# Kernel optimization log

Hardware: AMD Instinct MI355X
Metric: run time of the kernel (lower is better)

The kernel has to match this reference:

```python
import jax, jax.numpy as jnp
import numpy as np

# ---- fixed 16-atom graph topology from OrbECG.__init__ (flag_cg_global == 0) ----
EDGE1 = np.array([0, 0, 1, 2, 2, 3, 4, 5, 6, 8, 8, 9, 10, 11, 11, 13, 14])
EDGE2 = np.array([1, 4, 2, 3, 5, 4, 12, 6, 7, 9, 12, 10, 11, 12, 13, 14, 15])
EDGE_LIST = [[1, 4], [0, 2], [1, 3, 5], [2, 4], [0, 3, 12], [2, 6], [5, 7], [5, 6],
             [9, 12], [8, 10], [9, 11], [10, 12, 13], [4, 8, 11], [11, 14], [13, 15], [13, 14]]

def _build_pairs():
    eps, ni = [], []
    for node_idx, conn in enumerate(EDGE_LIST):
        for i in range(len(conn)):
            for j in range(i + 1, len(conn)):
                eps.append((conn[i], conn[j]))
                ni.append(node_idx)
    return np.array(eps), np.array(ni)

EDGE_PAIRS, NODE_IDX = _build_pairs()          # (24,2), (24,)
CROSS_SCALE = np.array([-0.25, 0.25], np.float32)
SIGMA_LIST = np.array([0.4, 0.8, 1.2], np.float32)
NUM_ATOMS = 16
N1 = NUM_ATOMS + len(EDGE1)                    # 33 (atoms + bond midpoints)
N2 = len(CROSS_SCALE) * len(EDGE_PAIRS)        # 48 cross points
BLOCK = N1 + N2                                # 81 per sigma block
NUM_BASIS = len(SIGMA_LIST) * BLOCK            # 243
NUM_BEADS = 8
NUM_ENC = 128
BATCH = 1024


def make_opposite_blocks(C):
    """Faithful to OrbECG.make_opposite_blocks: within each sigma block, the n2
    (cross-point) columns are tied in pairs: even col keeps gradient, odd col = -even (detached).
    All other columns come from a detached clone."""
    cols = jnp.arange(NUM_BASIS)
    bpos = cols % BLOCK
    off = bpos - N1
    even_mask = (bpos >= N1) & (off % 2 == 0)
    odd_mask = (bpos >= N1) & (off % 2 == 1)
    shifted = jnp.roll(C, 1, axis=-1)  # value at previous column (the paired even col)
    base = jax.lax.stop_gradient(C)
    out = jnp.where(even_mask, C, base)
    out = jnp.where(odd_mask, -jax.lax.stop_gradient(shifted), out)
    return out


def setup_inputs() -> dict:
    key = jax.random.key(0)
    ks = jax.random.split(key, 8)
    pos = jax.random.normal(ks[0], (BATCH, NUM_ATOMS, 3), jnp.float32)
    cg_ref = 0.01 * jax.random.normal(ks[1], (1, NUM_BEADS, NUM_BASIS), jnp.float32)
    sigma_param = jnp.zeros((len(SIGMA_LIST),), jnp.float32)
    # SoftEncoder(enc_ovl): num_bins=128, bin_min=-1, bin_max=1, sigma=0.2
    centers = jnp.linspace(-1.0, 1.0, NUM_ENC)[None, :].astype(jnp.float32)
    enc_weight = centers / (0.2 ** 2)
    enc_bias = -0.5 * (centers / 0.2) ** 2
    mu_proj = jnp.linspace(-2.5, 3.0, NUM_ENC)[:, None].astype(jnp.float32)
    lr_proj = jnp.array([3.5], jnp.float32)
    b = 1.0 / np.sqrt(NUM_ENC)
    def lin(k, o, i):
        k1, k2 = jax.random.split(k)
        return (jax.random.uniform(k1, (o, i), jnp.float32, -b, b),
                jax.random.uniform(k2, (o,), jnp.float32, -b, b))
    W1, b1 = lin(ks[2], NUM_ENC, NUM_ENC)
    W2, b2 = lin(ks[3], NUM_ENC, NUM_ENC)
    W3, b3 = lin(ks[4], NUM_ENC, NUM_ENC)
    return {"pos": pos, "cg_ref": cg_ref, "sigma_param": sigma_param,
            "enc_weight": enc_weight, "enc_bias": enc_bias, "mu_proj": mu_proj,
            "lr_proj": lr_proj, "W1": W1, "b1": b1, "W2": W2, "b2": b2, "W3": W3, "b3": b3}


def reference(pos, cg_ref, sigma_param, enc_weight, enc_bias, mu_proj, lr_proj,
              W1, b1, W2, b2, W3, b3):
    B = pos.shape[0]
    e1 = jnp.asarray(EDGE1); e2 = jnp.asarray(EDGE2)
    ep = jnp.asarray(EDGE_PAIRS); ni = jnp.asarray(NODE_IDX)
    # --- reference Gaussian centers: atoms, bond midpoints (basis_list=[0.5]), cross points ---
    atom = pos                                             # (B,16,3)
    bond = 0.5 * (pos[:, e1] + pos[:, e2])                 # (B,17,3)
    center = pos[:, ni]                                    # (B,24,3)
    diff = pos[:, ep[:, 0]] - pos[:, ep[:, 1]]             # (B,24,3)
    cross = center[:, :, None, :] + jnp.asarray(CROSS_SCALE)[None, None, :, None] * diff[:, :, None, :]
    pts_blk = jnp.concatenate([atom, bond, cross.reshape(B, N2, 3)], axis=1)  # (B,81,3)
    pts = jnp.tile(pts_blk, (1, len(SIGMA_LIST), 1))        # (B,243,3)
    sig = jnp.repeat(jnp.asarray(SIGMA_LIST) * jnp.exp(sigma_param), BLOCK)   # (243,)
    # --- pairwise Gaussian overlap matrix S (B,243,243) ---
    d2 = jnp.sum((pts[:, :, None, :] - pts[:, None, :, :]) ** 2, axis=-1)
    s2 = sig[:, None] ** 2 + sig[None, :] ** 2
    S = (2.0 * sig[:, None] * sig[None, :] / s2) ** 1.5 * jnp.exp(-d2 / (2.0 * s2))
    # --- bead-bead overlaps via CG coefficients (antisymmetrized cross columns) ---
    C = make_opposite_blocks(cg_ref[0])                     # (8,243)
    T = jnp.einsum('bij,qj->biq', S, C)
    ovl = jnp.einsum('pi,biq->bpq', C, T)                   # (B,8,8)
    # --- soft encode overlaps, MLP prediction, project onto mu grid ---
    x = ovl.reshape(-1, 1)                                  # (B*64,1)
    e = jax.nn.softmax(enc_weight * x + enc_bias, axis=1)   # (B*64,128)
    h = jax.nn.relu(e @ W1.T + b1)
    h = jax.nn.relu(h @ W2.T + b2)
    h = h @ W3.T + b3
    p = jax.nn.softmax(h, axis=1)
    mu = p @ mu_proj                                        # (B*64,1)
    return lr_proj[0] * mu.reshape(B, NUM_BEADS, NUM_BEADS)
```

## Files before the change

### kernel.cpp

```cpp
#include <hip/hip_runtime.h>

#define NT 256
#define NBATCH 1024
#define NOUT 65536

#if __has_builtin(__builtin_amdgcn_exp2f)
#define EXP2(x) __builtin_amdgcn_exp2f(x)
#else
#define EXP2(x) exp2f(x)
#endif

__constant__ int c_e1[17] = {0,0,1,2,2,3,4,5,6,8,8,9,10,11,11,13,14};
__constant__ int c_e2[17] = {1,4,2,3,5,4,12,6,7,9,12,10,11,12,13,14,15};
__constant__ int c_p0[24] = {1,0,1,1,3,2,0,0,3,2,5,5,9,8,9,10,10,12,4,4,8,11,13,13};
__constant__ int c_p1[24] = {4,2,3,5,5,4,3,12,12,6,7,6,12,10,11,11,13,13,8,11,11,14,15,14};
__constant__ int c_ni[24] = {0,1,2,2,2,3,4,4,4,5,6,7,8,9,10,11,11,11,12,12,12,13,14,15};

__constant__ int c_pa[6]   = {0,0,0,1,1,2};
__constant__ int c_pb[6]   = {0,1,2,1,2,2};
__constant__ int c_diag[6] = {1,0,0,1,0,1};

__global__ __launch_bounds__(256, 6)
void k_ovl(const float* __restrict__ pos, const float* __restrict__ cg,
           const float* __restrict__ sigp, float* __restrict__ xout,
           float* __restrict__ bmin, float* __restrict__ bmax) {
  __shared__ __align__(16) float smem[6216];
  float* posS          = smem;
  float (*P4)[4]       = (float(*)[4])   (smem + 48);
  float (*CT)[81][8]   = (float(*)[81][8])(smem + 372);
  float (*Vall)[81][8] = (float(*)[81][8])(smem + 2316);
  float* cInv          = smem + 6204;
  float* cLgp          = smem + 6210;
  float (*red16)[65]   = (float(*)[65])  (smem + 2316);

  const int b = blockIdx.x;
  const int t = threadIdx.x;

  if (t < 48) posS[t] = pos[b * 48 + t];

  for (int idx = t; idx < 3 * 81 * 8; idx += 256) {
    int s = idx / 648;
    int rem = idx - s * 648;
    int j = rem >> 3, q = rem & 7;
    int col = s * 81 + j;
    int off = j - 33;
    float v;
    if (off >= 0 && (off & 1)) v = -cg[q * 243 + (col - 1)];
    else                       v =  cg[q * 243 + col];
    CT[s][j][q] = v;
  }

  if (t == 0) {
    float sg[3];
    sg[0] = 0.4f * __expf(sigp[0]);
    sg[1] = 0.8f * __expf(sigp[1]);
    sg[2] = 1.2f * __expf(sigp[2]);
    #pragma unroll
    for (int p = 0; p < 6; ++p) {
      float sa = sg[c_pa[p]], sb = sg[c_pb[p]];
      float s2 = sa * sa + sb * sb;
      float rr = 2.0f * sa * sb / s2;
      cLgp[p] = 1.5f * __log2f(rr) - (float)c_diag[p];
      cInv[p] = (-0.5f / s2) * 1.44269504088896f;
    }
  }
  __syncthreads();

  if (t < 81) {
    float x, y, z;
    if (t < 16) {
      x = posS[t * 3]; y = posS[t * 3 + 1]; z = posS[t * 3 + 2];
    } else if (t < 33) {
      int e = t - 16;
      int a0 = c_e1[e] * 3, a1 = c_e2[e] * 3;
      x = 0.5f * (posS[a0] + posS[a1]);
      y = 0.5f * (posS[a0 + 1] + posS[a1 + 1]);
      z = 0.5f * (posS[a0 + 2] + posS[a1 + 2]);
    } else {
      int k = (t - 33) >> 1, sgn = (t - 33) & 1;
      float sc = sgn ? 0.25f : -0.25f;
      int n = c_ni[k] * 3, a0 = c_p0[k] * 3, a1 = c_p1[k] * 3;
      x = posS[n]     + sc * (posS[a0]     - posS[a1]);
      y = posS[n + 1] + sc * (posS[a0 + 1] - posS[a1 + 1]);
      z = posS[n + 2] + sc * (posS[a0 + 2] - posS[a1 + 2]);
    }
    P4[t][0] = x; P4[t][1] = y; P4[t][2] = z;
    P4[t][3] = x * x + y * y + z * z;
  }
  __syncthreads();

  if (t < 246) {
    const int s = t / 41;
    const int st = t - s * 41;
    const int i0 = st * 2;
    const bool two = (st < 40);
    const int i1 = two ? i0 + 1 : i0;
    const int bb = c_pb[s];
    const float nInv = cInv[s];
    const float lgp  = cLgp[s];

    const float4 pA = *(const float4*)P4[i0];
    const float4 pB = *(const float4*)P4[i1];
    const float cA = fmaf(pA.w, nInv, lgp);
    const float cB = fmaf(pB.w, nInv, lgp);
    const float m2 = -2.0f * nInv;

    float v00=0,v01=0,v02=0,v03=0,v04=0,v05=0,v06=0,v07=0;
    float v10=0,v11=0,v12=0,v13=0,v14=0,v15=0,v16=0,v17=0;

    #pragma unroll 3
    for (int j = 0; j < 33; ++j) {
      const float4 pj = *(const float4*)P4[j];
      const float rj = pj.w * nInv;
      const float dA = pA.x * pj.x + pA.y * pj.y + pA.z * pj.z;
      const float dB = pB.x * pj.x + pB.y * pj.y + pB.z * pj.z;
      const float eA = EXP2(fmaf(m2, dA, cA + rj));
      const float eB = EXP2(fmaf(m2, dB, cB + rj));
      const float4 cb0 = *(const float4*)&CT[bb][j][0];
      const float4 cb1 = *(const float4*)&CT[bb][j][4];
      v00 = fmaf(eA, cb0.x, v00); v01 = fmaf(eA, cb0.y, v01);
      v02 = fmaf(eA, cb0.z, v02); v03 = fmaf(eA, cb0.w, v03);
      v04 = fmaf(eA, cb1.x, v04); v05 = fmaf(eA, cb1.y, v05);
      v06 = fmaf(eA, cb1.z, v06); v07 = fmaf(eA, cb1.w, v07);
      v10 = fmaf(eB, cb0.x, v10); v11 = fmaf(eB, cb0.y, v11);
      v12 = fmaf(eB, cb0.z, v12); v13 = fmaf(eB, cb0.w, v13);
      v14 = fmaf(eB, cb1.x, v14); v15 = fmaf(eB, cb1.y, v15);
      v16 = fmaf(eB, cb1.z, v16); v17 = fmaf(eB, cb1.w, v17);
    }

    for (int k = 0; k < 24; ++k) {
      const int jp = 33 + (k << 1);
      const float4 pp = *(const float4*)P4[jp];
      const float4 pm = *(const float4*)P4[jp + 1];
      const float rp = pp.w * nInv;
      const float rm = pm.w * nInv;
      const float dAp = pA.x * pp.x + pA.y * pp.y + pA.z * pp.z;
      const float dBp = pB.x * pp.x + pB.y * pp.y + pB.z * pp.z;
      const float dAm = pA.x * pm.x + pA.y * pm.y + pA.z * pm.z;
      const float dBm = pB.x * pm.x + pB.y * pm.y + pB.z * pm.z;
      const float gA = EXP2(fmaf(m2, dAp, cA + rp)) - EXP2(fmaf(m2, dAm, cA + rm));
      const float gB = EXP2(fmaf(m2, dBp, cB + rp)) - EXP2(fmaf(m2, dBm, cB + rm));
      const float4 cb0 = *(const float4*)&CT[bb][jp][0];
      const float4 cb1 = *(const float4*)&CT[bb][jp][4];
      v00 = fmaf(gA, cb0.x, v00); v01 = fmaf(gA, cb0.y, v01);
      v02 = fmaf(gA, cb0.z, v02); v03 = fmaf(gA, cb0.w, v03);
      v04 = fmaf(gA, cb1.x, v04); v05 = fmaf(gA, cb1.y, v05);
      v06 = fmaf(gA, cb1.z, v06); v07 = fmaf(gA, cb1.w, v07);
      v10 = fmaf(gB, cb0.x, v10); v11 = fmaf(gB, cb0.y, v11);
      v12 = fmaf(gB, cb0.z, v12); v13 = fmaf(gB, cb0.w, v13);
      v14 = fmaf(gB, cb1.x, v14); v15 = fmaf(gB, cb1.y, v15);
      v16 = fmaf(gB, cb1.z, v16); v17 = fmaf(gB, cb1.w, v17);
    }

    float4* vo = (float4*)&Vall[s][i0][0];
    vo[0] = make_float4(v00, v01, v02, v03);
    vo[1] = make_float4(v04, v05, v06, v07);
    if (two) {
      vo[2] = make_float4(v10, v11, v12, v13);
      vo[3] = make_float4(v14, v15, v16, v17);
    }
  }
  __syncthreads();

  float w00=0,w01=0,w02=0,w03=0, w10=0,w11=0,w12=0,w13=0;
  float w20=0,w21=0,w22=0,w23=0, w30=0,w31=0,w32=0,w33=0;
  const int ch = t & 15;
  if (t < 64) {
    const int pg = (t >> 5) & 1;
    const int qg = (t >> 4) & 1;
    const int ib = ch * 5;
    const int ie = (ch == 15) ? 81 : ib + 5;
    #pragma unroll
    for (int s = 0; s < 6; ++s) {
      const int lf = c_pa[s];
      for (int i = ib; i < ie; ++i) {
        const float4 ct = *(const float4*)&CT[lf][i][pg * 4];
        const float4 vv = *(const float4*)&Vall[s][i][qg * 4];
        w00 = fmaf(ct.x, vv.x, w00); w01 = fmaf(ct.x, vv.y, w01);
        w02 = fmaf(ct.x, vv.z, w02); w03 = fmaf(ct.x, vv.w, w03);
        w10 = fmaf(ct.y, vv.x, w10); w11 = fmaf(ct.y, vv.y, w11);
        w12 = fmaf(ct.y, vv.z, w12); w13 = fmaf(ct.y, vv.w, w13);
        w20 = fmaf(ct.z, vv.x, w20); w21 = fmaf(ct.z, vv.y, w21);
        w22 = fmaf(ct.z, vv.z, w22); w23 = fmaf(ct.z, vv.w, w23);
        w30 = fmaf(ct.w, vv.x, w30); w31 = fmaf(ct.w, vv.y, w31);
        w32 = fmaf(ct.w, vv.z, w32); w33 = fmaf(ct.w, vv.w, w33);
      }
    }
  }
  __syncthreads();
  if (t < 64) {
    const int pg = (t >> 5) & 1;
    const int qg = (t >> 4) & 1;
    const int base = pg * 32 + qg * 4;
    red16[ch][base + 0 * 8 + 0] = w00; red16[ch][base + 0 * 8 + 1] = w01;
    red16[ch][base + 0 * 8 + 2] = w02; red16[ch][base + 0 * 8 + 3] = w03;
    red16[ch][base + 1 * 8 + 0] = w10; red16[ch][base + 1 * 8 + 1] = w11;
    red16[ch][base + 1 * 8 + 2] = w12; red16[ch][base + 1 * 8 + 3] = w13;
    red16[ch][base + 2 * 8 + 0] = w20; red16[ch][base + 2 * 8 + 1] = w21;
    red16[ch][base + 2 * 8 + 2] = w22; red16[ch][base + 2 * 8 + 3] = w23;
    red16[ch][base + 3 * 8 + 0] = w30; red16[ch][base + 3 * 8 + 1] = w31;
    red16[ch][base + 3 * 8 + 2] = w32; red16[ch][base + 3 * 8 + 3] = w33;
  }
  __syncthreads();

  if (t < 64) {
    float ws = 0.0f;
    #pragma unroll
    for (int c = 0; c < 16; ++c) ws += red16[c][t];
    const float sym = __shfl(ws, ((t & 7) << 3) | (t >> 3));
    const float v = ws + sym;
    xout[b * 64 + t] = v;
    float vmin = v, vmax = v;
    #pragma unroll
    for (int off = 32; off; off >>= 1) {
      vmin = fminf(vmin, __shfl_down(vmin, off));
      vmax = fmaxf(vmax, __shfl_down(vmax, off));
    }
    if (t == 0) { bmin[b] = vmin; bmax[b] = vmax; }
  }
}

__device__ __forceinline__ float dot128(const float* __restrict__ W,
                                        const float* __restrict__ act, int t) {
  const float4* w4 = (const float4*)(W + (size_t)t * 128);
  const float4* a4 = (const float4*)act;
  float acc = 0.0f;
  #pragma unroll
  for (int kq = 0; kq < 32; ++kq) {
    float4 w = w4[kq];
    float4 a = a4[kq];
    acc += w.x * a.x + w.y * a.y + w.z * a.z + w.w * a.w;
  }
  return acc;
}

__global__ __launch_bounds__(128)
void k_table(const float* __restrict__ ew, const float* __restrict__ eb,
             const float* __restrict__ mup, const float* __restrict__ lrp,
             const float* __restrict__ W1, const float* __restrict__ b1,
             const float* __restrict__ W2, const float* __restrict__ b2,
             const float* __restrict__ W3, const float* __restrict__ b3,
             const float* __restrict__ bmin, const float* __restrict__ bmax,
             float* __restrict__ mmf, float* __restrict__ table) {
  __shared__ __align__(16) float actA[128];
  __shared__ __align__(16) float actB[128];
  __shared__ float red[2];
  __shared__ float red2[2];
  const int t = threadIdx.x;
  const int wv = t >> 6;

  float mn = 1e30f, mx = -1e30f;
  #pragma unroll
  for (int i = 0; i < 8; ++i) {
    mn = fminf(mn, bmin[t + i * 128]);
    mx = fmaxf(mx, bmax[t + i * 128]);
  }
  #pragma unroll
  for (int off = 32; off; off >>= 1) {
    mn = fminf(mn, __shfl_xor(mn, off));
    mx = fmaxf(mx, __shfl_xor(mx, off));
  }
  if ((t & 63) == 0) { red[wv] = mn; red2[wv] = mx; }
  __syncthreads();
  const float xmin = fminf(red[0], red[1]);
  const float xmax = fmaxf(red2[0], red2[1]);
  if (blockIdx.x == 0 && t == 0) { mmf[0] = xmin; mmf[1] = xmax; }
  __syncthreads();

  const float x = xmin + (xmax - xmin) * ((float)blockIdx.x / (float)(NT - 1));

  float lg = ew[t] * x + eb[t];
  float m = lg;
  #pragma unroll
  for (int off = 32; off; off >>= 1) m = fmaxf(m, __shfl_xor(m, off));
  if ((t & 63) == 0) red[wv] = m;
  __syncthreads();
  m = fmaxf(red[0], red[1]);
  float ev = __expf(lg - m);
  float s = ev;
  #pragma unroll
  for (int off = 32; off; off >>= 1) s += __shfl_xor(s, off);
  if ((t & 63) == 0) red2[wv] = s;
  __syncthreads();
  s = red2[0] + red2[1];
  actA[t] = ev / s;
  __syncthreads();

  float h = fmaxf(b1[t] + dot128(W1, actA, t), 0.0f);
  actB[t] = h;
  __syncthreads();
  h = fmaxf(b2[t] + dot128(W2, actB, t), 0.0f);
  actA[t] = h;
  __syncthreads();
  float h3 = b3[t] + dot128(W3, actA, t);

  float m3 = h3;
  #pragma unroll
  for (int off = 32; off; off >>= 1) m3 = fmaxf(m3, __shfl_xor(m3, off));
  __syncthreads();
  if ((t & 63) == 0) red[wv] = m3;
  __syncthreads();
  m3 = fmaxf(red[0], red[1]);
  float e3 = __expf(h3 - m3);
  float dn = e3;
  float nm = e3 * mup[t];
  #pragma unroll
  for (int off = 32; off; off >>= 1) {
    dn += __shfl_xor(dn, off);
    nm += __shfl_xor(nm, off);
  }
  __syncthreads();
  if ((t & 63) == 0) { red[wv] = dn; red2[wv] = nm; }
  __syncthreads();
  if (t == 0)
    table[blockIdx.x] = lrp[0] * ((red2[0] + red2[1]) / (red[0] + red[1]));
}

__global__ __launch_bounds__(256)
void k_interp(const float* __restrict__ xbuf, const float* __restrict__ table,
              const float* __restrict__ mmf, float* __restrict__ out, int n) {
  const int r = blockIdx.x * 256 + threadIdx.x;
  if (r >= n) return;
  const float xmin = mmf[0];
  const float xmax = mmf[1];
  const float range = xmax - xmin;
  const float scale = (range > 0.0f) ? (float)(NT - 1) / range : 0.0f;
  float p = (xbuf[r] - xmin) * scale;
  int i0 = (int)floorf(p);
  i0 = min(max(i0, 0), NT - 2);
  const float w = p - (float)i0;
  out[r] = table[i0] + w * (table[i0 + 1] - table[i0]);
}

extern "C" void kernel_launch(void* const* d_in, const int* in_sizes, int n_in,
                              void* d_out, int out_size, void* d_ws, size_t ws_size,
                              hipStream_t stream) {
  const float* pos  = (const float*)d_in[0];
  const float* cg   = (const float*)d_in[1];
  const float* sigp = (const float*)d_in[2];
  const float* ew   = (const float*)d_in[3];
  const float* eb   = (const float*)d_in[4];
  const float* mup  = (const float*)d_in[5];
  const float* lrp  = (const float*)d_in[6];
  const float* W1   = (const float*)d_in[7];
  const float* b1   = (const float*)d_in[8];
  const float* W2   = (const float*)d_in[9];
  const float* b2   = (const float*)d_in[10];
  const float* W3   = (const float*)d_in[11];
  const float* b3   = (const float*)d_in[12];
  float* out = (float*)d_out;

  float* mmf   = (float*)d_ws;
  float* xbuf  = (float*)d_ws + 16;
  float* table = xbuf + NOUT;
  float* bmin  = table + NT;
  float* bmax  = bmin + NBATCH;

  k_ovl<<<NBATCH, 256, 0, stream>>>(pos, cg, sigp, xbuf, bmin, bmax);
  k_table<<<NT, 128, 0, stream>>>(ew, eb, mup, lrp, W1, b1, W2, b2, W3, b3,
                                  bmin, bmax, mmf, table);
  k_interp<<<(NOUT + 255) / 256, 256, 0, stream>>>(xbuf, table, mmf, out, NOUT);
}
```

Baseline: 38.60 us.

## Split overlap kernel across two blocks per batch with fp16 shared buffers

Each batch element is now handled by two blocks: one computes the atom/midpoint columns and the other the antisymmetric cross-point columns. Each block writes partial bead-overlap sums, which a new combine kernel adds, symmetrizes and reduces to min/max. The CG coefficients and intermediate V values are stored as fp16 in shared memory, halving LDS footprint to allow more resident blocks. This costs an extra kernel launch, a duplicated setup per block, and reduced precision in the contraction.

```diff
diff --git a/kernel.cpp b/kernel.cpp
--- a/kernel.cpp
+++ b/kernel.cpp
@@ -1,4 +1,5 @@
 #include <hip/hip_runtime.h>
+#include <hip/hip_fp16.h>
 
 #define NT 256
 #define NBATCH 1024
@@ -20,20 +21,32 @@
 __constant__ int c_pb[6]   = {0,1,2,1,2,2};
 __constant__ int c_diag[6] = {1,0,0,1,0,1};
 
+static __device__ __forceinline__ unsigned pk2(float a, float b) {
+  __half ha = __float2half(a), hb = __float2half(b);
+  unsigned ua = *reinterpret_cast<unsigned short*>(&ha);
+  unsigned ub = *reinterpret_cast<unsigned short*>(&hb);
+  return ua | (ub << 16);
+}
+static __device__ __forceinline__ float2 up2(unsigned u) {
+  __half2 h = *reinterpret_cast<__half2*>(&u);
+  return __half22float2(h);
+}
+
 __global__ __launch_bounds__(256, 6)
 void k_ovl(const float* __restrict__ pos, const float* __restrict__ cg,
-           const float* __restrict__ sigp, float* __restrict__ xout,
-           float* __restrict__ bmin, float* __restrict__ bmax) {
-  __shared__ __align__(16) float smem[6216];
-  float* posS          = smem;
-  float (*P4)[4]       = (float(*)[4])   (smem + 48);
-  float (*CT)[81][8]   = (float(*)[81][8])(smem + 372);
-  float (*Vall)[81][8] = (float(*)[81][8])(smem + 2316);
-  float* cInv          = smem + 6204;
-  float* cLgp          = smem + 6210;
-  float (*red16)[65]   = (float(*)[65])  (smem + 2316);
-
-  const int b = blockIdx.x;
+           const float* __restrict__ sigp, float* __restrict__ wpart) {
+  __shared__ __align__(16) float smem[3300];
+  float* posS        = smem;
+  float (*P4)[4]     = (float(*)[4])(smem + 48);
+  __half (*CTh)[81][8] = (__half(*)[81][8])(smem + 372);
+  __half (*Vh)[81][8]  = (__half(*)[81][8])(smem + 1344);
+  float (*red16)[65] = (float(*)[65])(smem + 1344);
+  float* cInv        = smem + 3288;
+  float* cLgp        = smem + 3294;
+
+  const int bid = blockIdx.x;
+  const int b = bid >> 1;
+  const int h = bid & 1;
   const int t = threadIdx.x;
 
   if (t < 48) posS[t] = pos[b * 48 + t];
@@ -47,7 +60,7 @@
     float v;
     if (off >= 0 && (off & 1)) v = -cg[q * 243 + (col - 1)];
     else                       v =  cg[q * 243 + col];
-    CT[s][j][q] = v;
+    ((__half*)CTh)[idx] = __float2half(v);
   }
 
   if (t == 0) {
@@ -108,56 +121,62 @@
     float v00=0,v01=0,v02=0,v03=0,v04=0,v05=0,v06=0,v07=0;
     float v10=0,v11=0,v12=0,v13=0,v14=0,v15=0,v16=0,v17=0;
 
-    #pragma unroll 3
-    for (int j = 0; j < 33; ++j) {
-      const float4 pj = *(const float4*)P4[j];
-      const float rj = pj.w * nInv;
-      const float dA = pA.x * pj.x + pA.y * pj.y + pA.z * pj.z;
-      const float dB = pB.x * pj.x + pB.y * pj.y + pB.z * pj.z;
-      const float eA = EXP2(fmaf(m2, dA, cA + rj));
-      const float eB = EXP2(fmaf(m2, dB, cB + rj));
-      const float4 cb0 = *(const float4*)&CT[bb][j][0];
-      const float4 cb1 = *(const float4*)&CT[bb][j][4];
-      v00 = fmaf(eA, cb0.x, v00); v01 = fmaf(eA, cb0.y, v01);
-      v02 = fmaf(eA, cb0.z, v02); v03 = fmaf(eA, cb0.w, v03);
-      v04 = fmaf(eA, cb1.x, v04); v05 = fmaf(eA, cb1.y, v05);
-      v06 = fmaf(eA, cb1.z, v06); v07 = fmaf(eA, cb1.w, v07);
-      v10 = fmaf(eB, cb0.x, v10); v11 = fmaf(eB, cb0.y, v11);
-      v12 = fmaf(eB, cb0.z, v12); v13 = fmaf(eB, cb0.w, v13);
-      v14 = fmaf(eB, cb1.x, v14); v15 = fmaf(eB, cb1.y, v15);
-      v16 = fmaf(eB, cb1.z, v16); v17 = fmaf(eB, cb1.w, v17);
-    }
-
-    for (int k = 0; k < 24; ++k) {
-      const int jp = 33 + (k << 1);
-      const float4 pp = *(const float4*)P4[jp];
-      const float4 pm = *(const float4*)P4[jp + 1];
-      const float rp = pp.w * nInv;
-      const float rm = pm.w * nInv;
-      const float dAp = pA.x * pp.x + pA.y * pp.y + pA.z * pp.z;
-      const float dBp = pB.x * pp.x + pB.y * pp.y + pB.z * pp.z;
-      const float dAm = pA.x * pm.x + pA.y * pm.y + pA.z * pm.z;
-      const float dBm = pB.x * pm.x + pB.y * pm.y + pB.z * pm.z;
-      const float gA = EXP2(fmaf(m2, dAp, cA + rp)) - EXP2(fmaf(m2, dAm, cA + rm));
-      const float gB = EXP2(fmaf(m2, dBp, cB + rp)) - EXP2(fmaf(m2, dBm, cB + rm));
-      const float4 cb0 = *(const float4*)&CT[bb][jp][0];
-      const float4 cb1 = *(const float4*)&CT[bb][jp][4];
-      v00 = fmaf(gA, cb0.x, v00); v01 = fmaf(gA, cb0.y, v01);
-      v02 = fmaf(gA, cb0.z, v02); v03 = fmaf(gA, cb0.w, v03);
-      v04 = fmaf(gA, cb1.x, v04); v05 = fmaf(gA, cb1.y, v05);
-      v06 = fmaf(gA, cb1.z, v06); v07 = fmaf(gA, cb1.w, v07);
-      v10 = fmaf(gB, cb0.x, v10); v11 = fmaf(gB, cb0.y, v11);
-      v12 = fmaf(gB, cb0.z, v12); v13 = fmaf(gB, cb0.w, v13);
-      v14 = fmaf(gB, cb1.x, v14); v15 = fmaf(gB, cb1.y, v15);
-      v16 = fmaf(gB, cb1.z, v16); v17 = fmaf(gB, cb1.w, v17);
-    }
-
-    float4* vo = (float4*)&Vall[s][i0][0];
-    vo[0] = make_float4(v00, v01, v02, v03);
-    vo[1] = make_float4(v04, v05, v06, v07);
+    if (h == 0) {
+      for (int j = 0; j < 33; ++j) {
+        const float4 pj = *(const float4*)P4[j];
+        const float rj = pj.w * nInv;
+        const float dA = pA.x * pj.x + pA.y * pj.y + pA.z * pj.z;
+        const float dB = pB.x * pj.x + pB.y * pj.y + pB.z * pj.z;
+        const float eA = EXP2(fmaf(m2, dA, cA + rj));
+        const float eB = EXP2(fmaf(m2, dB, cB + rj));
+        const uint4 cu = *(const uint4*)&CTh[bb][j][0];
+        const float2 c01 = up2(cu.x), c23 = up2(cu.y);
+        const float2 c45 = up2(cu.z), c67 = up2(cu.w);
+        v00 = fmaf(eA, c01.x, v00); v01 = fmaf(eA, c01.y, v01);
+        v02 = fmaf(eA, c23.x, v02); v03 = fmaf(eA, c23.y, v03);
+        v04 = fmaf(eA, c45.x, v04); v05 = fmaf(eA, c45.y, v05);
+        v06 = fmaf(eA, c67.x, v06); v07 = fmaf(eA, c67.y, v07);
+        v10 = fmaf(eB, c01.x, v10); v11 = fmaf(eB, c01.y, v11);
+        v12 = fmaf(eB, c23.x, v12); v13 = fmaf(eB, c23.y, v13);
+        v14 = fmaf(eB, c45.x, v14); v15 = fmaf(eB, c45.y, v15);
+        v16 = fmaf(eB, c67.x, v16); v17 = fmaf(eB, c67.y, v17);
+      }
+    } else {
+      for (int k = 0; k < 24; ++k) {
+        const int jp = 33 + (k << 1);
+        const float4 pp = *(const float4*)P4[jp];
+        const float4 pm = *(const float4*)P4[jp + 1];
+        const float rp = pp.w * nInv;
+        const float rm = pm.w * nInv;
+        const float dAp = pA.x * pp.x + pA.y * pp.y + pA.z * pp.z;
+        const float dBp = pB.x * pp.x + pB.y * pp.y + pB.z * pp.z;
+        const float dAm = pA.x * pm.x + pA.y * pm.y + pA.z * pm.z;
+        const float dBm = pB.x * pm.x + pB.y * pm.y + pB.z * pm.z;
+        const float gA = EXP2(fmaf(m2, dAp, cA + rp)) - EXP2(fmaf(m2, dAm, cA + rm));
+        const float gB = EXP2(fmaf(m2, dBp, cB + rp)) - EXP2(fmaf(m2, dBm, cB + rm));
+        const uint4 cu = *(const uint4*)&CTh[bb][jp][0];
+        const float2 c01 = up2(cu.x), c23 = up2(cu.y);
+        const float2 c45 = up2(cu.z), c67 = up2(cu.w);
+        v00 = fmaf(gA, c01.x, v00); v01 = fmaf(gA, c01.y, v01);
+        v02 = fmaf(gA, c23.x, v02); v03 = fmaf(gA, c23.y, v03);
+        v04 = fmaf(gA, c45.x, v04); v05 = fmaf(gA, c45.y, v05);
+        v06 = fmaf(gA, c67.x, v06); v07 = fmaf(gA, c67.y, v07);
+        v10 = fmaf(gB, c01.x, v10); v11 = fmaf(gB, c01.y, v11);
+        v12 = fmaf(gB, c23.x, v12); v13 = fmaf(gB, c23.y, v13);
+        v14 = fmaf(gB, c45.x, v14); v15 = fmaf(gB, c45.y, v15);
+        v16 = fmaf(gB, c67.x, v16); v17 = fmaf(gB, c67.y, v17);
+      }
+    }
+
+    uint4 r0;
+    r0.x = pk2(v00, v01); r0.y = pk2(v02, v03);
+    r0.z = pk2(v04, v05); r0.w = pk2(v06, v07);
+    *(uint4*)&Vh[s][i0][0] = r0;
     if (two) {
-      vo[2] = make_float4(v10, v11, v12, v13);
-      vo[3] = make_float4(v14, v15, v16, v17);
+      uint4 r1;
+      r1.x = pk2(v10, v11); r1.y = pk2(v12, v13);
+      r1.z = pk2(v14, v15); r1.w = pk2(v16, v17);
+      *(uint4*)&Vh[s][i0 + 1][0] = r1;
     }
   }
   __syncthreads();
@@ -174,16 +193,18 @@
     for (int s = 0; s < 6; ++s) {
       const int lf = c_pa[s];
       for (int i = ib; i < ie; ++i) {
-        const float4 ct = *(const float4*)&CT[lf][i][pg * 4];
-        const float4 vv = *(const float4*)&Vall[s][i][qg * 4];
-        w00 = fmaf(ct.x, vv.x, w00); w01 = fmaf(ct.x, vv.y, w01);
-        w02 = fmaf(ct.x, vv.z, w02); w03 = fmaf(ct.x, vv.w, w03);
-        w10 = fmaf(ct.y, vv.x, w10); w11 = fmaf(ct.y, vv.y, w11);
-        w12 = fmaf(ct.y, vv.z, w12); w13 = fmaf(ct.y, vv.w, w13);
-        w20 = fmaf(ct.z, vv.x, w20); w21 = fmaf(ct.z, vv.y, w21);
-        w22 = fmaf(ct.z, vv.z, w22); w23 = fmaf(ct.z, vv.w, w23);
-        w30 = fmaf(ct.w, vv.x, w30); w31 = fmaf(ct.w, vv.y, w31);
-        w32 = fmaf(ct.w, vv.z, w32); w33 = fmaf(ct.w, vv.w, w33);
+        const uint2 cu = *(const uint2*)&CTh[lf][i][pg * 4];
+        const float2 a01 = up2(cu.x), a23 = up2(cu.y);
+        const uint2 vu = *(const uint2*)&Vh[s][i][qg * 4];
+        const float2 b01 = up2(vu.x), b23 = up2(vu.y);
+        w00 = fmaf(a01.x, b01.x, w00); w01 = fmaf(a01.x, b01.y, w01);
+        w02 = fmaf(a01.x, b23.x, w02); w03 = fmaf(a01.x, b23.y, w03);
+        w10 = fmaf(a01.y, b01.x, w10); w11 = fmaf(a01.y, b01.y, w11);
+        w12 = fmaf(a01.y, b23.x, w12); w13 = fmaf(a01.y, b23.y, w13);
+        w20 = fmaf(a23.x, b01.x, w20); w21 = fmaf(a23.x, b01.y, w21);
+        w22 = fmaf(a23.x, b23.x, w22); w23 = fmaf(a23.x, b23.y, w23);
+        w30 = fmaf(a23.y, b01.x, w30); w31 = fmaf(a23.y, b01.y, w31);
+        w32 = fmaf(a23.y, b23.x, w32); w33 = fmaf(a23.y, b23.y, w33);
       }
     }
   }
@@ -207,16 +228,33 @@
     float ws = 0.0f;
     #pragma unroll
     for (int c = 0; c < 16; ++c) ws += red16[c][t];
-    const float sym = __shfl(ws, ((t & 7) << 3) | (t >> 3));
-    const float v = ws + sym;
-    xout[b * 64 + t] = v;
-    float vmin = v, vmax = v;
-    #pragma unroll
-    for (int off = 32; off; off >>= 1) {
-      vmin = fminf(vmin, __shfl_down(vmin, off));
-      vmax = fmaxf(vmax, __shfl_down(vmax, off));
-    }
-    if (t == 0) { bmin[b] = vmin; bmax[b] = vmax; }
+    wpart[(size_t)bid * 64 + t] = ws;
+  }
+}
+
+__global__ __launch_bounds__(256)
+void k_combine(const float* __restrict__ wpart, float* __restrict__ xbuf,
+               float* __restrict__ bmin, float* __restrict__ bmax) {
+  __shared__ float rmn[4], rmx[4];
+  const int t = threadIdx.x;
+  const int idx = blockIdx.x * 256 + t;
+  const int b = idx >> 6;
+  const int e = idx & 63;
+  const int eT = ((e & 7) << 3) | (e >> 3);
+  const float* wa = wpart + (size_t)b * 128;
+  const float v = wa[e] + wa[64 + e] + wa[eT] + wa[64 + eT];
+  xbuf[idx] = v;
+  float mn = v, mx = v;
+  #pragma unroll
+  for (int off = 32; off; off >>= 1) {
+    mn = fminf(mn, __shfl_xor(mn, off));
+    mx = fmaxf(mx, __shfl_xor(mx, off));
+  }
+  if ((t & 63) == 0) { rmn[t >> 6] = mn; rmx[t >> 6] = mx; }
+  __syncthreads();
+  if (t == 0) {
+    bmin[blockIdx.x] = fminf(fminf(rmn[0], rmn[1]), fminf(rmn[2], rmn[3]));
+    bmax[blockIdx.x] = fmaxf(fmaxf(rmx[0], rmx[1]), fmaxf(rmx[2], rmx[3]));
   }
 }
 
@@ -249,12 +287,8 @@
   const int t = threadIdx.x;
   const int wv = t >> 6;
 
-  float mn = 1e30f, mx = -1e30f;
-  #pragma unroll
-  for (int i = 0; i < 8; ++i) {
-    mn = fminf(mn, bmin[t + i * 128]);
-    mx = fmaxf(mx, bmax[t + i * 128]);
-  }
+  float mn = fminf(bmin[t], bmin[t + 128]);
+  float mx = fmaxf(bmax[t], bmax[t + 128]);
   #pragma unroll
   for (int off = 32; off; off >>= 1) {
     mn = fminf(mn, __shfl_xor(mn, off));
@@ -354,9 +388,11 @@
   float* xbuf  = (float*)d_ws + 16;
   float* table = xbuf + NOUT;
   float* bmin  = table + NT;
-  float* bmax  = bmin + NBATCH;
-
-  k_ovl<<<NBATCH, 256, 0, stream>>>(pos, cg, sigp, xbuf, bmin, bmax);
+  float* bmax  = bmin + 256;
+  float* wpart = bmax + 256;
+
+  k_ovl<<<2 * NBATCH, 256, 0, stream>>>(pos, cg, sigp, wpart);
+  k_combine<<<NOUT / 256, 256, 0, stream>>>(wpart, xbuf, bmin, bmax);
   k_table<<<NT, 128, 0, stream>>>(ew, eb, mup, lrp, W1, b1, W2, b2, W3, b3,
                                   bmin, bmax, mmf, table);
   k_interp<<<(NOUT + 255) / 256, 256, 0, stream>>>(xbuf, table, mmf, out, NOUT);
```

New measurement: 46.65 us. 1.21x slower.
